# Optimization experiments

Measured on AMD Instinct MI355X. Metric: run time of the kernel, lower is better.

Reference implementation:

```python
import jax, jax.numpy as jnp
import numpy as np

G, NPG, MAXN = 1024, 40, 51   # graphs, nodes/graph, dense pad size
EPG = 80                       # edges per graph
N, E = G * NPG, G * EPG
D_IN, D_OUT, D_EDGE = 64, 32, 16


def _lin(key, fan_in, shape):
    b = 1.0 / np.sqrt(fan_in)
    return jax.random.uniform(key, shape, jnp.float32, -b, b)


def setup_inputs() -> dict:
    key = jax.random.key(0)
    ks = jax.random.split(key, 24)
    node_features = jax.random.randint(ks[0], (N, 9), 0, 128)
    edge_features = jax.random.randint(ks[1], (E, 3), 0, 8)
    offs = jnp.repeat(jnp.arange(G) * NPG, EPG)
    src = jax.random.randint(ks[2], (E,), 0, NPG) + offs
    dst = jax.random.randint(ks[3], (E,), 0, NPG) + offs
    edge_index = jnp.stack([src, dst])
    batch = jnp.repeat(jnp.arange(G), NPG)
    inp = dict(node_features=node_features, edge_features=edge_features,
               edge_index=edge_index, batch=batch)
    # OGB-style encoders: one embedding table per feature column, summed
    inp['atom_emb'] = jax.random.normal(ks[4], (9, 128, D_IN), jnp.float32) * 0.1
    inp['bond_emb'] = jax.random.normal(ks[5], (3, 8, D_EDGE), jnp.float32) * 0.1
    # edge-conditioned weight MLP: 16 -> 1024 -> 256 -> 64*32 (no bias)
    inp['gW1'] = _lin(ks[6], 16, (16, 1024))
    inp['gW2'] = _lin(ks[7], 1024, (1024, 256))
    inp['gW3'] = _lin(ks[8], 256, (256, D_IN * D_OUT))
    # NNConv root weight + bias
    inp['root'] = _lin(ks[9], D_IN, (D_IN, D_OUT))
    inp['conv_bias'] = jnp.zeros((D_OUT,), jnp.float32)
    # readout MLP: 51*32 -> 256 -> 128 -> 32 -> 8 -> 1
    dims = [MAXN * D_OUT, 256, 128, 32, 8, 1]
    for i in range(5):
        inp[f'mW{i+1}'] = _lin(ks[10 + 2 * i], dims[i], (dims[i], dims[i + 1]))
        inp[f'mb{i+1}'] = _lin(ks[11 + 2 * i], dims[i], (dims[i + 1],))
    return inp


def reference(node_features, edge_features, edge_index, batch,
              atom_emb, bond_emb, gW1, gW2, gW3, root, conv_bias,
              mW1, mb1, mW2, mb2, mW3, mb3, mW4, mb4, mW5, mb5):
    # encoders: sum of per-column embeddings
    x = jnp.sum(atom_emb[jnp.arange(9), node_features], axis=1)      # [N,64]
    e = jnp.sum(bond_emb[jnp.arange(3), edge_features], axis=1)      # [E,16]
    # per-edge weight matrix via MLP
    h = jax.nn.relu(e @ gW1)
    h = jax.nn.relu(h @ gW2)
    w = (h @ gW3).reshape(-1, D_IN, D_OUT)                           # [E,64,32]
    # NNConv: gather src, per-edge matmul, scatter-add to dst, + root + bias
    src, dst = edge_index[0], edge_index[1]
    msg = jnp.einsum('ed,edo->eo', x[src], w)                        # [E,32]
    agg = jax.ops.segment_sum(msg, dst, num_segments=N)              # [N,32]
    out = agg + x @ root + conv_bias
    # to_dense_batch(max_num_nodes=51); exactly NPG nodes per graph, zero-pad
    dense = jnp.zeros((G, MAXN, D_OUT), out.dtype).at[:, :NPG].set(
        out.reshape(G, NPG, D_OUT))
    f = dense.reshape(G, MAXN * D_OUT)                               # [G,1632]
    f = jax.nn.relu(f @ mW1 + mb1)
    f = jax.nn.relu(f @ mW2 + mb2)
    f = jax.nn.relu(f @ mW3 + mb3)
    f = jax.nn.relu(f @ mW4 + mb4)
    return f @ mW5 + mb5                                             # [G,1]
```

## Files before the change

kernel.cpp:

```cpp
#include <hip/hip_runtime.h>

#define NNODES 40960
#define NEDGES 81920
#define NG     1024
#define NCOMBO 512
#define NHB    320
#define NGRP   4

__global__ __launch_bounds__(256) void k_node(
    const int* __restrict__ nf, const float* __restrict__ emb,
    const float* __restrict__ root, const float* __restrict__ bias,
    float* __restrict__ x, float* __restrict__ out) {
    __shared__ float sx[4][64];
    const int t = threadIdx.x;
    const int ln = t >> 6;
    const int d  = t & 63;
    const int n  = blockIdx.x * 4 + ln;
    const int* nfr = nf + n * 9;
    float acc = 0.f;
#pragma unroll
    for (int c = 0; c < 9; ++c) {
        int idx = nfr[c];
        acc += emb[((c << 7) + idx) * 64 + d];
    }
    x[n * 64 + d] = acc;
    sx[ln][d] = acc;
    __syncthreads();
    if (d < 32) {
        float o = bias[d];
#pragma unroll
        for (int k = 0; k < 64; ++k) o += sx[ln][k] * root[k * 32 + d];
        out[n * 32 + d] = o;
    }
}

__global__ __launch_bounds__(256) void k_h1(
    const float* __restrict__ bemb, const float* __restrict__ gW1,
    float* __restrict__ h1) {
    __shared__ float se[16];
    const int b = blockIdx.x, t = threadIdx.x;
    const int c = b >> 2;
    const int n = ((b & 3) << 8) + t;
    if (t < 16) {
        int f0 = c >> 6, f1 = (c >> 3) & 7, f2 = c & 7;
        se[t] = bemb[f0 * 16 + t] + bemb[(8 + f1) * 16 + t] +
                bemb[(16 + f2) * 16 + t];
    }
    __syncthreads();
    float acc = 0.f;
#pragma unroll
    for (int k = 0; k < 16; ++k) acc += se[k] * gW1[k * 1024 + n];
    h1[c * 1024 + n] = fmaxf(acc, 0.f);
}

__global__ void k_hist(const int* __restrict__ ef, int* __restrict__ cid,
                       int* __restrict__ bh) {
    __shared__ int lh[512];
    const int t = threadIdx.x, b = blockIdx.x;
    lh[t] = 0; lh[t + 256] = 0;
    __syncthreads();
    int e = b * 256 + t;
    int c = (ef[e * 3] << 6) | (ef[e * 3 + 1] << 3) | ef[e * 3 + 2];
    cid[e] = c;
    atomicAdd(&lh[c], 1);
    __syncthreads();
    bh[b * 512 + t]       = lh[t];
    bh[b * 512 + 256 + t] = lh[t + 256];
}

__global__ __launch_bounds__(512) void k_scan(int* __restrict__ bh,
                                              int* __restrict__ offs) {
    __shared__ int tmp[512];
    const int c = threadIdx.x;
    int s = 0;
    for (int b = 0; b < NHB; ++b) {
        int v = bh[b * 512 + c];
        bh[b * 512 + c] = s;
        s += v;
    }
    tmp[c] = s;
    __syncthreads();
    for (int d = 1; d < 512; d <<= 1) {
        int add = (c >= d) ? tmp[c - d] : 0;
        __syncthreads();
        tmp[c] += add;
        __syncthreads();
    }
    int excl = tmp[c] - s;
    offs[c] = excl;
    if (c == 511) offs[512] = tmp[511];
    for (int b = 0; b < NHB; ++b) bh[b * 512 + c] += excl;
}

__global__ void k_scatter(const int* __restrict__ cid, const int* __restrict__ src,
                          const int* __restrict__ dst, const int* __restrict__ bh,
                          int2* __restrict__ esd) {
    __shared__ int cur[512];
    const int t = threadIdx.x, b = blockIdx.x;
    cur[t]       = bh[b * 512 + t];
    cur[t + 256] = bh[b * 512 + 256 + t];
    __syncthreads();
    int e = b * 256 + t;
    int p = atomicAdd(&cur[cid[e]], 1);
    esd[p] = make_int2(src[e], dst[e]);
}

template <int BM, int BN, int BK, int TM, int TN>
__global__ __launch_bounds__(256)
void k_gemm_tiled(const float* __restrict__ A, const float* __restrict__ B,
                  const float* __restrict__ bias, float* __restrict__ C,
                  float* __restrict__ Cp, int M, int N, int K, int KS, int relu) {
    constexpr int TX = BN / TN;
    constexpr int TY = BM / TM;
    static_assert(TX * TY == 256, "block must be 256 threads");
    __shared__ float As[BK][BM + 4];
    __shared__ float Bs[BK][BN + 4];
    const int tx = threadIdx.x % TX, ty = threadIdx.x / TX;
    const int row0 = blockIdx.y * BM, col0 = blockIdx.x * BN;
    const int z = blockIdx.z;
    const int k_begin = z * KS, k_end = k_begin + KS;

    const int am = threadIdx.x >> 2;
    const int ak = (threadIdx.x & 3) << 2;
    const int bk = threadIdx.x >> 4;
    const int bn = (threadIdx.x & 15) << 2;

    float acc[TM][TN] = {};
    for (int k0 = k_begin; k0 < k_end; k0 += BK) {
        float4 av = *reinterpret_cast<const float4*>(&A[(row0 + am) * K + k0 + ak]);
        float4 bv = *reinterpret_cast<const float4*>(&B[(k0 + bk) * N + col0 + bn]);
        As[ak + 0][am] = av.x;
        As[ak + 1][am] = av.y;
        As[ak + 2][am] = av.z;
        As[ak + 3][am] = av.w;
        *reinterpret_cast<float4*>(&Bs[bk][bn]) = bv;
        __syncthreads();
#pragma unroll
        for (int k = 0; k < BK; ++k) {
            float a[TM], b[TN];
            *reinterpret_cast<float4*>(a) =
                *reinterpret_cast<const float4*>(&As[k][ty * TM]);
            *reinterpret_cast<float4*>(b) =
                *reinterpret_cast<const float4*>(&Bs[k][tx * TN]);
#pragma unroll
            for (int i = 0; i < TM; ++i)
#pragma unroll
                for (int j = 0; j < TN; ++j) acc[i][j] += a[i] * b[j];
        }
        __syncthreads();
    }

    const int MN = M * N;
    if (gridDim.z == 1) {
#pragma unroll
        for (int i = 0; i < TM; ++i) {
            int r = row0 + ty * TM + i;
            float4 v;
            v.x = acc[i][0]; v.y = acc[i][1]; v.z = acc[i][2]; v.w = acc[i][3];
            int c = col0 + tx * TN;
            if (bias) { v.x += bias[c]; v.y += bias[c+1]; v.z += bias[c+2]; v.w += bias[c+3]; }
            if (relu) { v.x = fmaxf(v.x,0.f); v.y = fmaxf(v.y,0.f);
                        v.z = fmaxf(v.z,0.f); v.w = fmaxf(v.w,0.f); }
            *reinterpret_cast<float4*>(&C[r * N + c]) = v;
        }
    } else {
        float* dstp = Cp + z * MN;
#pragma unroll
        for (int i = 0; i < TM; ++i) {
            int r = row0 + ty * TM + i;
            float4 v;
            v.x = acc[i][0]; v.y = acc[i][1]; v.z = acc[i][2]; v.w = acc[i][3];
            *reinterpret_cast<float4*>(&dstp[r * N + col0 + tx * TN]) = v;
        }
    }
}

__global__ void k_reduceK(const float* __restrict__ Cp, const float* __restrict__ bias,
                          float* __restrict__ C, int MN, int N, int nz, int relu) {
    int i4 = (blockIdx.x * 256 + threadIdx.x) * 4;
    if (i4 >= MN) return;
    float4 acc = *reinterpret_cast<const float4*>(&Cp[i4]);
    for (int z = 1; z < nz; ++z) {
        float4 t = *reinterpret_cast<const float4*>(&Cp[z * MN + i4]);
        acc.x += t.x; acc.y += t.y; acc.z += t.z; acc.w += t.w;
    }
    if (bias) {
        int c = i4 % N;
        acc.x += bias[c]; acc.y += bias[c + 1]; acc.z += bias[c + 2]; acc.w += bias[c + 3];
    }
    if (relu) {
        acc.x = fmaxf(acc.x, 0.f); acc.y = fmaxf(acc.y, 0.f);
        acc.z = fmaxf(acc.z, 0.f); acc.w = fmaxf(acc.w, 0.f);
    }
    *reinterpret_cast<float4*>(&C[i4]) = acc;
}

__global__ __launch_bounds__(256) void k_msgg(
    const float* __restrict__ x, const float* __restrict__ wtab,
    const int* __restrict__ offs, const int2* __restrict__ esd,
    float* __restrict__ out) {
    const int c   = blockIdx.x >> 2;
    const int grp = blockIdx.x & 3;
    const int t = threadIdx.x;
    const int o = t & 31, slot = t >> 5;
    const int e0 = offs[c];
    const int n_c = offs[c + 1] - e0;
    if (grp * 64 >= n_c) return;

    __shared__ float swT[32][65];
    __shared__ float sx[64][64];
    __shared__ int ssrc[64], sdst[64];

#pragma unroll
    for (int j = 0; j < 8; ++j) {
        int i = t + j * 256;
        swT[i & 31][i >> 5] = wtab[c * 2048 + i];
    }
    __syncthreads();
    float wr[64];
#pragma unroll
    for (int k = 0; k < 64; ++k) wr[k] = swT[o][k];

    for (int base = grp * 64; base < n_c; base += NGRP * 64) {
        int n_e = min(64, n_c - base);
        __syncthreads();
        if (t < n_e) {
            int2 sd = esd[e0 + base + t];
            ssrc[t] = sd.x; sdst[t] = sd.y;
        }
        __syncthreads();
#pragma unroll
        for (int i = 0; i < 16; ++i) {
            int idx = t + i * 256;
            int r = idx >> 6, d = idx & 63;
            if (r < n_e) sx[r][d] = x[ssrc[r] * 64 + d];
        }
        __syncthreads();
#pragma unroll
        for (int j = 0; j < 8; ++j) {
            int ei = slot * 8 + j;
            if (ei < n_e) {
                const float4* xv = reinterpret_cast<const float4*>(sx[ei]);
                float acc = 0.f;
#pragma unroll
                for (int k4 = 0; k4 < 16; ++k4) {
                    float4 xq = xv[k4];
                    acc += xq.x * wr[k4 * 4 + 0];
                    acc += xq.y * wr[k4 * 4 + 1];
                    acc += xq.z * wr[k4 * 4 + 2];
                    acc += xq.w * wr[k4 * 4 + 3];
                }
                atomicAdd(&out[sdst[ei] * 32 + o], acc);
            }
        }
    }
}

__global__ __launch_bounds__(256) void k_tail2(
    const float* __restrict__ f1,
    const float* __restrict__ mW2, const float* __restrict__ mb2,
    const float* __restrict__ mW3, const float* __restrict__ mb3,
    const float* __restrict__ mW4, const float* __restrict__ mb4,
    const float* __restrict__ mW5, const float* __restrict__ mb5,
    float* __restrict__ outv) {
    __shared__ float s1[4][256];
    __shared__ float s2[4][128];
    __shared__ float s3[4][32];
    __shared__ float s4[4][8];
    const int t  = threadIdx.x;
    const int g0 = blockIdx.x * 4;
#pragma unroll
    for (int i = 0; i < 4; ++i) {
        int idx = t + i * 256;
        s1[idx >> 8][idx & 255] = f1[g0 * 256 + idx];
    }
    __syncthreads();
#pragma unroll
    for (int i = 0; i < 2; ++i) {
        int idx = t + i * 256;
        int g = idx >> 7, cc = idx & 127;
        float acc = mb2[cc];
#pragma unroll 8
        for (int k = 0; k < 256; ++k) acc += s1[g][k] * mW2[k * 128 + cc];
        s2[g][cc] = fmaxf(acc, 0.f);
    }
    __syncthreads();
    const int w = t >> 6, lane = t & 63;
    if (lane < 32) {
        float acc = mb3[lane];
#pragma unroll 8
        for (int k = 0; k < 128; ++k) acc += s2[w][k] * mW3[k * 32 + lane];
        s3[w][lane] = fmaxf(acc, 0.f);
    }
    __syncthreads();
    if (lane < 8) {
        float acc = mb4[lane];
#pragma unroll
        for (int k = 0; k < 32; ++k) acc += s3[w][k] * mW4[k * 8 + lane];
        s4[w][lane] = fmaxf(acc, 0.f);
    }
    __syncthreads();
    if (lane == 0) {
        float acc = mb5[0];
#pragma unroll
        for (int k = 0; k < 8; ++k) acc += s4[w][k] * mW5[k];
        outv[g0 + w] = acc;
    }
}

extern "C" void kernel_launch(void* const* d_in, const int* in_sizes, int n_in,
                              void* d_out, int out_size, void* d_ws, size_t ws_size,
                              hipStream_t stream) {
    const int*   nf      = (const int*)d_in[0];
    const int*   ef      = (const int*)d_in[1];
    const int*   eidx    = (const int*)d_in[2];
    const float* atom_emb= (const float*)d_in[4];
    const float* bond_emb= (const float*)d_in[5];
    const float* gW1     = (const float*)d_in[6];
    const float* gW2     = (const float*)d_in[7];
    const float* gW3     = (const float*)d_in[8];
    const float* root    = (const float*)d_in[9];
    const float* cbias   = (const float*)d_in[10];
    const float* mW1     = (const float*)d_in[11];
    const float* mb1     = (const float*)d_in[12];
    const float* mW2     = (const float*)d_in[13];
    const float* mb2     = (const float*)d_in[14];
    const float* mW3     = (const float*)d_in[15];
    const float* mb3     = (const float*)d_in[16];
    const float* mW4     = (const float*)d_in[17];
    const float* mb4     = (const float*)d_in[18];
    const float* mW5     = (const float*)d_in[19];
    const float* mb5     = (const float*)d_in[20];

    const int* src = eidx;
    const int* dst = eidx + NEDGES;

    float* ws = (float*)d_ws;
    float* x    = ws;
    float* out  = x + 2621440;
    float* h1   = out + 1310720;
    float* h2   = h1 + 524288;
    float* wtab = h2 + 131072;
    float* f1   = wtab + 1048576;
    float* part = f1 + 262144;
    int*   cid  = (int*)(part + 2097152);
    int*   bh   = cid + 81920;
    int*   offs = bh + 163840;
    int2*  esd  = (int2*)(offs + 1024);

    k_node<<<NNODES / 4, 256, 0, stream>>>(nf, atom_emb, root, cbias, x, out);
    k_hist<<<NHB, 256, 0, stream>>>(ef, cid, bh);
    k_scan<<<1, 512, 0, stream>>>(bh, offs);
    k_scatter<<<NHB, 256, 0, stream>>>(cid, src, dst, bh, esd);
    k_h1<<<NCOMBO * 4, 256, 0, stream>>>(bond_emb, gW1, h1);
    k_gemm_tiled<64, 64, 16, 4, 4><<<dim3(4, 8, 16), 256, 0, stream>>>(
        h1, gW2, nullptr, nullptr, part, NCOMBO, 256, 1024, 64, 0);
    k_reduceK<<<131072 / 1024, 256, 0, stream>>>(part, nullptr, h2, 131072, 256, 16, 1);
    k_gemm_tiled<64, 64, 16, 4, 4><<<dim3(32, 8, 2), 256, 0, stream>>>(
        h2, gW3, nullptr, nullptr, part, NCOMBO, 2048, 256, 128, 0);
    k_reduceK<<<1048576 / 1024, 256, 0, stream>>>(part, nullptr, wtab, 1048576, 2048, 2, 0);
    k_msgg<<<NCOMBO * NGRP, 256, 0, stream>>>(x, wtab, offs, esd, out);
    k_gemm_tiled<64, 64, 16, 4, 4><<<dim3(4, 16, 8), 256, 0, stream>>>(
        out, mW1, nullptr, nullptr, part, NG, 256, 1280, 160, 0);
    k_reduceK<<<262144 / 1024, 256, 0, stream>>>(part, mb1, f1, 262144, 256, 8, 1);
    k_tail2<<<NG / 4, 256, 0, stream>>>(f1, mW2, mb2, mW3, mb3, mW4, mb4,
                                        mW5, mb5, (float*)d_out);
}
```

Baseline: 268.4 us.

## Parallelize counting-sort scan across combos with two-level block scan

Replaces the single-block serial scan over 320 histogram blocks with a two-level scan. The histogram is now stored combo-major, one block per combo scans its per-block counts, and a second small kernel scans the combo totals. The scatter kernel adds the combo offset when it initializes its cursors. This removes a long serial loop of dependent global reads and writes run by only 512 threads, at the cost of one extra launch and transposed, strided histogram writes.

```diff
diff --git a/kernel.cpp b/kernel.cpp
--- a/kernel.cpp
+++ b/kernel.cpp
@@ -64,41 +64,51 @@
     cid[e] = c;
     atomicAdd(&lh[c], 1);
     __syncthreads();
-    bh[b * 512 + t]       = lh[t];
-    bh[b * 512 + 256 + t] = lh[t + 256];
-}
-
-__global__ __launch_bounds__(512) void k_scan(int* __restrict__ bh,
-                                              int* __restrict__ offs) {
+    bh[t * NHB + b]         = lh[t];
+    bh[(t + 256) * NHB + b] = lh[t + 256];
+}
+
+__global__ __launch_bounds__(512) void k_scanA(int* __restrict__ bh,
+                                               int* __restrict__ tot) {
     __shared__ int tmp[512];
-    const int c = threadIdx.x;
-    int s = 0;
-    for (int b = 0; b < NHB; ++b) {
-        int v = bh[b * 512 + c];
-        bh[b * 512 + c] = s;
-        s += v;
-    }
-    tmp[c] = s;
+    const int c = blockIdx.x, t = threadIdx.x;
+    int v = (t < NHB) ? bh[c * NHB + t] : 0;
+    tmp[t] = v;
     __syncthreads();
     for (int d = 1; d < 512; d <<= 1) {
-        int add = (c >= d) ? tmp[c - d] : 0;
-        __syncthreads();
-        tmp[c] += add;
-        __syncthreads();
-    }
-    int excl = tmp[c] - s;
-    offs[c] = excl;
-    if (c == 511) offs[512] = tmp[511];
-    for (int b = 0; b < NHB; ++b) bh[b * 512 + c] += excl;
+        int add = (t >= d) ? tmp[t - d] : 0;
+        __syncthreads();
+        tmp[t] += add;
+        __syncthreads();
+    }
+    if (t < NHB) bh[c * NHB + t] = tmp[t] - v;
+    if (t == 511) tot[c] = tmp[511];
+}
+
+__global__ __launch_bounds__(512) void k_scanB(const int* __restrict__ tot,
+                                               int* __restrict__ offs) {
+    __shared__ int tmp[512];
+    const int t = threadIdx.x;
+    int v = tot[t];
+    tmp[t] = v;
+    __syncthreads();
+    for (int d = 1; d < 512; d <<= 1) {
+        int add = (t >= d) ? tmp[t - d] : 0;
+        __syncthreads();
+        tmp[t] += add;
+        __syncthreads();
+    }
+    offs[t] = tmp[t] - v;
+    if (t == 511) offs[512] = tmp[511];
 }
 
 __global__ void k_scatter(const int* __restrict__ cid, const int* __restrict__ src,
                           const int* __restrict__ dst, const int* __restrict__ bh,
-                          int2* __restrict__ esd) {
+                          const int* __restrict__ offs, int2* __restrict__ esd) {
     __shared__ int cur[512];
     const int t = threadIdx.x, b = blockIdx.x;
-    cur[t]       = bh[b * 512 + t];
-    cur[t + 256] = bh[b * 512 + 256 + t];
+    cur[t]       = bh[t * NHB + b]         + offs[t];
+    cur[t + 256] = bh[(t + 256) * NHB + b] + offs[t + 256];
     __syncthreads();
     int e = b * 256 + t;
     int p = atomicAdd(&cur[cid[e]], 1);
@@ -345,13 +355,15 @@
     float* part = f1 + 262144;
     int*   cid  = (int*)(part + 2097152);
     int*   bh   = cid + 81920;
-    int*   offs = bh + 163840;
+    int*   tot  = bh + 163840;
+    int*   offs = tot + 512;
     int2*  esd  = (int2*)(offs + 1024);
 
     k_node<<<NNODES / 4, 256, 0, stream>>>(nf, atom_emb, root, cbias, x, out);
     k_hist<<<NHB, 256, 0, stream>>>(ef, cid, bh);
-    k_scan<<<1, 512, 0, stream>>>(bh, offs);
-    k_scatter<<<NHB, 256, 0, stream>>>(cid, src, dst, bh, esd);
+    k_scanA<<<NCOMBO, 512, 0, stream>>>(bh, tot);
+    k_scanB<<<1, 512, 0, stream>>>(tot, offs);
+    k_scatter<<<NHB, 256, 0, stream>>>(cid, src, dst, bh, offs, esd);
     k_h1<<<NCOMBO * 4, 256, 0, stream>>>(bond_emb, gW1, h1);
     k_gemm_tiled<64, 64, 16, 4, 4><<<dim3(4, 8, 16), 256, 0, stream>>>(
         h1, gW2, nullptr, nullptr, part, NCOMBO, 256, 1024, 64, 0);
```

Result: faster. 237.0 us (-11.7%).
